# Performance work log

Hardware: AMD Instinct MI355X
Metric: run time of the kernel (lower is better)

## Reference

```python
import jax, jax.numpy as jnp
import numpy as np

PRE_TOPK = 10000   # hardcoded score.topk(10000) in the torch module
TOPK = 100         # final detections kept per image
IOU_THR = 0.7


def cxcywh_to_xyxy(b):
    cx, cy, w, h = jnp.split(b, 4, axis=-1)
    return jnp.concatenate([cx - 0.5 * w, cy - 0.5 * h, cx + 0.5 * w, cy + 0.5 * h], axis=-1)


def iou_one_vs_all(box, boxes):
    # box: [4], boxes: [N,4] (xyxy). torchvision box_iou semantics (no degenerate clamp on areas).
    lt = jnp.maximum(box[:2], boxes[:, :2])
    rb = jnp.minimum(box[2:], boxes[:, 2:])
    wh = jnp.clip(rb - lt, 0.0)
    inter = wh[:, 0] * wh[:, 1]
    a1 = (box[2] - box[0]) * (box[3] - box[1])
    a2 = (boxes[:, 2] - boxes[:, 0]) * (boxes[:, 3] - boxes[:, 1])
    return inter / (a1 + a2 - inter)


def nms_keep_single(boxes, scores, labels):
    # batched (class-wise) NMS via the coordinate-offset trick, then greedy suppression.
    # boxes [N,4], scores [N], labels [N] int. Returns indices of kept boxes, [TOPK],
    # in descending-score order (matches torchvision batched_nms + [:topk]).
    offset = labels.astype(boxes.dtype) * (boxes.max() + 1.0)
    obox = boxes + offset[:, None]

    def step(live, _):
        i = jnp.argmax(live)                      # highest remaining score
        iou = iou_one_vs_all(obox[i], obox)       # [N]
        live = jnp.where(iou > IOU_THR, -jnp.inf, live)  # suppress (includes self, iou=1)
        return live, i

    _, keep = jax.lax.scan(step, scores, None, length=TOPK)
    return keep


def setup_inputs() -> dict:
    key = jax.random.key(0)
    k1, k2, k3 = jax.random.split(key, 3)
    pred_logits = jax.random.normal(k1, (8, 900, 91), dtype=jnp.float32)
    pred_boxes = jax.random.uniform(k2, (8, 900, 4), dtype=jnp.float32)  # cxcywh in [0,1]
    # realistic (h, w) image sizes ~ [600, 1400]
    target_sizes = 600.0 + 800.0 * jax.random.uniform(k3, (8, 2), dtype=jnp.float32)
    return {"pred_logits": pred_logits, "pred_boxes": pred_boxes, "target_sizes": target_sizes}


def reference(pred_logits, pred_boxes, target_sizes):
    bs, nq, nc = pred_logits.shape
    prob = jax.nn.sigmoid(pred_logits).reshape(bs, nq * nc)
    # pre-topk 10000 over flattened (query, class) scores
    top_scores, top_idx = jax.lax.top_k(prob, PRE_TOPK)   # [bs, PRE_TOPK]
    box_idx = top_idx // nc
    labels = top_idx % nc

    xyxy = cxcywh_to_xyxy(pred_boxes)                     # [bs, nq, 4]
    img_h, img_w = target_sizes[:, 0], target_sizes[:, 1]
    scale = jnp.stack([img_w, img_h, img_w, img_h], axis=1)  # [bs, 4]
    xyxy = xyxy * scale[:, None, :]
    boxes = jnp.take_along_axis(xyxy, box_idx[..., None], axis=1)  # [bs, PRE_TOPK, 4]

    keep = jax.vmap(nms_keep_single)(boxes, top_scores, labels)    # [bs, TOPK]

    out_scores = jnp.take_along_axis(top_scores, keep, axis=1)
    out_labels = jnp.take_along_axis(labels, keep, axis=1)
    out_boxes = jnp.take_along_axis(boxes, keep[..., None], axis=1)
    return out_scores, out_labels, out_boxes
```

## Files before the change

kernel.cpp:

```cpp
#include <hip/hip_runtime.h>
#include <cstdint>
#include <cstddef>

#define NQ 900
#define NC 91
#define NFLAT (NQ * NC)
#define NF4 (NFLAT / 4)
#define BS 8
#define PRE_TOPK 10000
#define TOPK 100
#define IOU_THR 0.7f
#define NT 1024
#define NWAVES 16
#define NCAND 256
#define HEADZ 2.55078125f
#define HEADCAP 768

__device__ __forceinline__ unsigned int mono_u(float z) {
    unsigned int b = __float_as_uint(z);
    return b ^ ((unsigned int)((int)b >> 31) | 0x80000000u);
}
__device__ __forceinline__ float inv_mono(unsigned int u) {
    unsigned int b = (u & 0x80000000u) ? (u ^ 0x80000000u) : ~u;
    return __uint_as_float(b);
}
__device__ __forceinline__ unsigned long long make_key(unsigned int u, int i) {
    return ((unsigned long long)u << 17) | (unsigned long long)(131071 - i);
}

extern "C" __global__ __launch_bounds__(NT)
void k_fused(const float* __restrict__ logits,
             const float* __restrict__ pboxes,
             const float* __restrict__ tsizes,
             float* __restrict__ out) {
    __shared__ unsigned long long sPool[PRE_TOPK];
    __shared__ unsigned long long sSup[1024];
    __shared__ float4 sBox[NQ];
    __shared__ unsigned long long sHead[HEADCAP];
    __shared__ unsigned long long sTop[NCAND];
    __shared__ float4 sOB[NCAND];
    __shared__ float sOar[NCAND];
    __shared__ unsigned long long sKeepW[4];
    __shared__ float sKx1[TOPK], sKy1[TOPK], sKx2[TOPK], sKy2[TOPK], sKa[TOPK];
    __shared__ float sFirst[6];
    __shared__ float sRedF[NWAVES];
    __shared__ int sWTot[NWAVES], sWSuf[NWAVES];
    __shared__ int sFlag, sKept, sPos, sNK, sHC;
    __shared__ float sBmax;

    const int b = blockIdx.x;
    const int tid = threadIdx.x;
    const int wid = tid >> 6, lane = tid & 63;
    const float* lg = logits + (size_t)b * NFLAT;
    const float* bx = pboxes + (size_t)b * NQ * 4;
    const float img_h = tsizes[b * 2 + 0], img_w = tsizes[b * 2 + 1];
    const unsigned long long laneLT = (1ULL << lane) - 1ULL;

    if (tid < HEADCAP) sHead[tid] = 0ULL;
    if (tid == 0) { sFlag = 0; sKept = 0; sPos = 0; sNK = 0; sHC = 0; }
    {
        float lmax = -3.4e38f;
        if (tid < NQ) {
            const float4 bb = ((const float4*)bx)[tid];
            float4 sb;
            sb.x = (bb.x - 0.5f * bb.z) * img_w;
            sb.y = (bb.y - 0.5f * bb.w) * img_h;
            sb.z = (bb.x + 0.5f * bb.z) * img_w;
            sb.w = (bb.y + 0.5f * bb.w) * img_h;
            sBox[tid] = sb;
            lmax = fmaxf(fmaxf(sb.x, sb.y), fmaxf(sb.z, sb.w));
        }
        for (int off = 32; off >= 1; off >>= 1)
            lmax = fmaxf(lmax, __shfl_xor(lmax, off, 64));
        if (lane == 0) sRedF[wid] = lmax;
    }
    __syncthreads();

    for (int jj = 0; jj < 5; ++jj) {
        float4 v[4]; bool hv[4];
        #pragma unroll
        for (int u = 0; u < 4; ++u) {
            const int j = tid + (4 * jj + u) * NT;
            hv[u] = (j < NF4);
            v[u] = ((const float4*)lg)[hv[u] ? j : (NF4 - 1)];
        }
        #pragma unroll
        for (int u = 0; u < 4; ++u) {
            const int j = tid + (4 * jj + u) * NT;
            const bool c0 = hv[u] && (v[u].x >= HEADZ);
            const bool c1 = hv[u] && (v[u].y >= HEADZ);
            const bool c2 = hv[u] && (v[u].z >= HEADZ);
            const bool c3 = hv[u] && (v[u].w >= HEADZ);
            const unsigned long long m0 = __ballot(c0), m1 = __ballot(c1),
                                     m2 = __ballot(c2), m3 = __ballot(c3);
            const int p0 = __popcll(m0), p1 = __popcll(m1), p2 = __popcll(m2);
            const int n = p0 + p1 + p2 + __popcll(m3);
            int base = 0;
            if (lane == 0 && n) base = atomicAdd(&sHC, n);
            base = __shfl(base, 0, 64);
            if (c0) { const int o = base + __popcll(m0 & laneLT);
                      if (o < HEADCAP) sHead[o] = make_key(mono_u(v[u].x), 4 * j); }
            if (c1) { const int o = base + p0 + __popcll(m1 & laneLT);
                      if (o < HEADCAP) sHead[o] = make_key(mono_u(v[u].y), 4 * j + 1); }
            if (c2) { const int o = base + p0 + p1 + __popcll(m2 & laneLT);
                      if (o < HEADCAP) sHead[o] = make_key(mono_u(v[u].z), 4 * j + 2); }
            if (c3) { const int o = base + p0 + p1 + p2 + __popcll(m3 & laneLT);
                      if (o < HEADCAP) sHead[o] = make_key(mono_u(v[u].w), 4 * j + 3); }
        }
    }
    __syncthreads();

    {
        const int hcRaw = sHC;
        if (tid == 0 && (hcRaw < NCAND || hcRaw > HEADCAP)) sFlag = 1;
        const int hc = hcRaw < HEADCAP ? hcRaw : HEADCAP;
        if (tid < hc) {
            const unsigned long long k = sHead[tid];
            int r = 0;
            const int hp = (hc + 7) & ~7;
            for (int q = 0; q < hp; q += 8) {
                #pragma unroll
                for (int u = 0; u < 8; ++u) r += (sHead[q + u] > k) ? 1 : 0;
            }
            if (r < NCAND) sTop[r] = k;
        }
    }
    __syncthreads();
    int bad = sFlag;

    if (!bad && tid < NCAND) {
        float mm = sRedF[0];
        #pragma unroll
        for (int q = 1; q < NWAVES; ++q) mm = fmaxf(mm, sRedF[q]);
        const unsigned long long k = sTop[tid];
        const int i = 131071 - (int)(k & 0x1FFFFULL);
        const int bi = i / NC, l = i - bi * NC;
        const float4 sb = sBox[bi];
        const float o = (float)l * (mm + 1.0f);
        float4 ob;
        ob.x = sb.x + o; ob.y = sb.y + o; ob.z = sb.z + o; ob.w = sb.w + o;
        sOB[tid] = ob;
        sOar[tid] = (ob.z - ob.x) * (ob.w - ob.y);
    }
    __syncthreads();

    if (!bad) {
        const int w = wid & 3;
        const int r0 = (wid >> 2) << 6;
        const int cj = (w << 6) + lane;
        const float4 cb = sOB[cj];
        const float car = sOar[cj];
        for (int t = 0; t < 64; ++t) {
            const int i = r0 + t;
            const float4 rb = sOB[i];
            const float ra = sOar[i];
            float iw = fminf(rb.z, cb.z) - fmaxf(rb.x, cb.x);
            float ih = fminf(rb.w, cb.w) - fmaxf(rb.y, cb.y);
            iw = fmaxf(iw, 0.f); ih = fmaxf(ih, 0.f);
            const float inter = iw * ih;
            const bool sup = inter > IOU_THR * (ra + car - inter);
            const unsigned long long bits = __ballot(sup);
            if (lane == 0) sSup[(i << 2) | w] = bits;
        }
    }
    __syncthreads();

    if (!bad && wid == 0) {
        unsigned long long live = (lane < 4) ? ~0ULL : 0ULL;
        unsigned long long keepW = 0ULL;
        int kept = 0;
        const int myw = lane & 3;
        for (int ch = 0; ch < 4 && kept < TOPK; ++ch) {
            unsigned long long cur = __shfl(live, ch, 64);
            unsigned long long acc = 0ULL;
            #pragma unroll 8
            for (int bit = 0; bit < 64; ++bit) {
                const int i = (ch << 6) | bit;
                const unsigned long long rowC = sSup[(i << 2) | ch];
                const unsigned long long rowM = sSup[(i << 2) | myw];
                if ((cur >> bit) & 1ULL) {
                    cur &= ~rowC;
                    acc |= rowM;
                    if (lane == ch) keepW |= 1ULL << bit;
                }
            }
            if (lane < 4) live &= ~acc;
            int c = __popcll(keepW);
            for (int off = 32; off >= 1; off >>= 1) c += __shfl_xor(c, off, 64);
            kept = c;
        }
        if (lane < 4) sKeepW[lane] = keepW;
        if (lane == 0) sNK = kept;
    }
    __syncthreads();
    if (tid == 0 && sFlag == 0) {
        if (sNK < TOPK) sFlag = 1; else sKept = TOPK;
    }
    __syncthreads();
    bad = sFlag;

    if (!bad && tid < NCAND) {
        const int w = tid >> 6;
        const unsigned long long m = sKeepW[w];
        if ((m >> (tid & 63)) & 1ULL) {
            int rank = __popcll(m & ((1ULL << (tid & 63)) - 1ULL));
            for (int ww = 0; ww < w; ++ww) rank += __popcll(sKeepW[ww]);
            if (rank < TOPK) {
                const unsigned long long k = sTop[tid];
                const int i = 131071 - (int)(k & 0x1FFFFULL);
                const int bi = i / NC, l = i - bi * NC;
                const float4 sb = sBox[bi];
                const float z = inv_mono((unsigned int)(k >> 17));
                const int oi = b * TOPK + rank;
                out[oi] = 1.0f / (1.0f + expf(-z));
                out[BS * TOPK + oi] = (float)l;
                out[2 * BS * TOPK + oi * 4 + 0] = sb.x;
                out[2 * BS * TOPK + oi * 4 + 1] = sb.y;
                out[2 * BS * TOPK + oi * 4 + 2] = sb.z;
                out[2 * BS * TOPK + oi * 4 + 3] = sb.w;
            }
        }
    }

    if (bad) {
        unsigned long long lo = 0, hi = (1ULL << 49) - 1;
        while (lo < hi) {
            const unsigned long long mid = lo + ((hi - lo + 1) >> 1);
            int c = 0;
            for (int j = tid; j < NF4; j += NT) {
                const float4 v = ((const float4*)lg)[j];
                const float zv[4] = { v.x, v.y, v.z, v.w };
                #pragma unroll
                for (int q = 0; q < 4; ++q)
                    c += (make_key(mono_u(zv[q]), 4 * j + q) >= mid) ? 1 : 0;
            }
            for (int off = 32; off >= 1; off >>= 1) c += __shfl_xor(c, off, 64);
            if (lane == 0) sWTot[wid] = c;
            __syncthreads();
            if (tid == 0) {
                int a = 0;
                for (int w = 0; w < NWAVES; ++w) a += sWTot[w];
                sPos = a;
            }
            __syncthreads();
            if (sPos >= PRE_TOPK) lo = mid; else hi = mid - 1;
            __syncthreads();
        }
        if (tid == 0) sPos = 0;
        __syncthreads();
        for (int j = tid; j < NF4; j += NT) {
            const float4 v = ((const float4*)lg)[j];
            const float zv[4] = { v.x, v.y, v.z, v.w };
            #pragma unroll
            for (int q = 0; q < 4; ++q) {
                const unsigned long long k = make_key(mono_u(zv[q]), 4 * j + q);
                const bool cand = k >= lo;
                const unsigned long long mask = __ballot(cand);
                int pos = 0;
                if (lane == 0 && mask) pos = atomicAdd(&sPos, __popcll(mask));
                pos = __shfl(pos, 0, 64);
                if (cand) sPool[pos + __popcll(mask & laneLT)] = k;
            }
        }
        __syncthreads();
        {
            unsigned long long stash[10]; int spp[10]; int ns = 0;
            for (int p = tid; p < PRE_TOPK; p += NT) {
                const unsigned long long k = sPool[p];
                int r = 0;
                for (int q = 0; q < PRE_TOPK; ++q) r += (sPool[q] > k) ? 1 : 0;
                if (ns < 10) { stash[ns] = k; spp[ns] = r; ++ns; }
            }
            __syncthreads();
            for (int q = 0; q < ns; ++q) sPool[spp[q]] = stash[q];
        }
        __syncthreads();
        float lmax = -3.4e38f;
        for (int p = tid; p < PRE_TOPK; p += NT) {
            const int i = 131071 - (int)(sPool[p] & 0x1FFFFULL);
            const float4 sb = sBox[i / NC];
            lmax = fmaxf(lmax, fmaxf(fmaxf(sb.x, sb.y), fmaxf(sb.z, sb.w)));
        }
        for (int off = 32; off >= 1; off >>= 1)
            lmax = fmaxf(lmax, __shfl_xor(lmax, off, 64));
        if (lane == 0) sRedF[wid] = lmax;
        __syncthreads();
        if (tid == 0) {
            float mm = sRedF[0];
            for (int k2 = 1; k2 < NWAVES; ++k2) mm = fmaxf(mm, sRedF[k2]);
            sBmax = mm;
        }
        __syncthreads();
        const float offc = sBmax + 1.0f;
        if (wid == 0) {
            int kept = 0;
            for (int base = 0; base < PRE_TOPK && kept < TOPK; base += 64) {
                const int c = base + lane;
                const bool valid = c < PRE_TOPK;
                const unsigned long long k = valid ? sPool[c] : 0ULL;
                const int i = valid ? (131071 - (int)(k & 0x1FFFFULL)) : 0;
                const int bi = i / NC, l = i - bi * NC;
                const float4 sb = sBox[bi];
                const float o = (float)l * offc;
                const float ox1 = sb.x + o, oy1 = sb.y + o, ox2 = sb.z + o, oy2 = sb.w + o;
                const float ar = (ox2 - ox1) * (oy2 - oy1);
                bool alive = valid;
                for (int jj = 0; jj < kept; ++jj) {
                    float iw = fminf(sKx2[jj], ox2) - fmaxf(sKx1[jj], ox1);
                    float ih = fminf(sKy2[jj], oy2) - fmaxf(sKy1[jj], oy1);
                    iw = fmaxf(iw, 0.f); ih = fmaxf(ih, 0.f);
                    const float inter = iw * ih;
                    if (inter > IOU_THR * (sKa[jj] + ar - inter)) alive = false;
                }
                unsigned long long mask = __ballot(alive);
                while (mask != 0ULL && kept < TOPK) {
                    const int s = __ffsll((unsigned long long)mask) - 1;
                    const float px1 = __shfl(ox1, s, 64);
                    const float py1 = __shfl(oy1, s, 64);
                    const float px2 = __shfl(ox2, s, 64);
                    const float py2 = __shfl(oy2, s, 64);
                    const float pa  = __shfl(ar,  s, 64);
                    if (lane == s) {
                        sKx1[kept] = ox1; sKy1[kept] = oy1; sKx2[kept] = ox2;
                        sKy2[kept] = oy2; sKa[kept] = ar;
                        const int oi = b * TOPK + kept;
                        const float z = inv_mono((unsigned int)(k >> 17));
                        const float sc = 1.0f / (1.0f + expf(-z));
                        out[oi] = sc;
                        out[BS * TOPK + oi] = (float)l;
                        out[2 * BS * TOPK + oi * 4 + 0] = sb.x;
                        out[2 * BS * TOPK + oi * 4 + 1] = sb.y;
                        out[2 * BS * TOPK + oi * 4 + 2] = sb.z;
                        out[2 * BS * TOPK + oi * 4 + 3] = sb.w;
                        if (kept == 0) { sFirst[0] = sc; sFirst[1] = (float)l;
                                         sFirst[2] = sb.x; sFirst[3] = sb.y;
                                         sFirst[4] = sb.z; sFirst[5] = sb.w; }
                    }
                    ++kept;
                    if (alive) {
                        float iw = fminf(px2, ox2) - fmaxf(px1, ox1);
                        float ih = fminf(py2, oy2) - fmaxf(py1, oy1);
                        iw = fmaxf(iw, 0.f); ih = fmaxf(ih, 0.f);
                        const float inter = iw * ih;
                        if (inter > IOU_THR * (pa + ar - inter)) alive = false;
                    }
                    mask = __ballot(alive);
                }
            }
            if (lane == 0) sKept = kept;
        }
        __syncthreads();
    }

    for (int t = sKept + tid; t < TOPK; t += NT) {
        const int oi = b * TOPK + t;
        out[oi] = sFirst[0];
        out[BS * TOPK + oi] = sFirst[1];
        out[2 * BS * TOPK + oi * 4 + 0] = sFirst[2];
        out[2 * BS * TOPK + oi * 4 + 1] = sFirst[3];
        out[2 * BS * TOPK + oi * 4 + 2] = sFirst[4];
        out[2 * BS * TOPK + oi * 4 + 3] = sFirst[5];
    }
}

extern "C" void kernel_launch(void* const* d_in, const int* in_sizes, int n_in,
                              void* d_out, int out_size, void* d_ws, size_t ws_size,
                              hipStream_t stream) {
    const float* logits = (const float*)d_in[0];
    const float* pboxes = (const float*)d_in[1];
    const float* ts     = (const float*)d_in[2];
    (void)d_ws; (void)ws_size;
    hipLaunchKernelGGL(k_fused, dim3(BS), dim3(NT), 0, stream,
                       logits, pboxes, ts, (float*)d_out);
}
```

Measured before the change: 91.37 us.

## Split logit threshold sweep into a separate multi-block kernel across slices

Moves the full pass over the 8x81900 logits out of the single-block-per-image kernel into a pre-kernel that uses 32 slices per image (256 blocks). Each slice compacts above-threshold keys into workspace, and the tail kernel prefix-sums the slice counts and gathers the keys into the head buffer. This spreads the memory-bound sweep over many CUs instead of 8, at the cost of an extra launch and a workspace round trip. If workspace is missing or a slice overflows, it falls back to the existing bad path.

```diff
diff --git a/kernel.cpp b/kernel.cpp
--- a/kernel.cpp
+++ b/kernel.cpp
@@ -15,6 +15,13 @@
 #define NCAND 256
 #define HEADZ 2.55078125f
 #define HEADCAP 768
+#define NSL 32
+#define SLCAP 64
+#define K1T 256
+
+#define CNT_OFF 0
+#define KEY_OFF 1024
+#define WS_REQ ((size_t)KEY_OFF + (size_t)BS * NSL * SLCAP * 8)
 
 __device__ __forceinline__ unsigned int mono_u(float z) {
     unsigned int b = __float_as_uint(z);
@@ -28,11 +35,53 @@
     return ((unsigned long long)u << 17) | (unsigned long long)(131071 - i);
 }
 
+extern "C" __global__ __launch_bounds__(K1T)
+void k_sweep(const float* __restrict__ logits, void* __restrict__ ws) {
+    __shared__ unsigned long long keys[SLCAP];
+    __shared__ int cnt;
+    const int sl = blockIdx.x, b = blockIdx.y;
+    const int tid = threadIdx.x, lane = tid & 63;
+    const unsigned long long laneLT = (1ULL << lane) - 1ULL;
+    if (tid == 0) cnt = 0;
+    __syncthreads();
+    const float* lg = logits + (size_t)b * NFLAT;
+    const int j0 = (sl * NF4) / NSL, j1 = ((sl + 1) * NF4) / NSL;
+    for (int j = j0 + tid; j < j1; j += K1T) {
+        const float4 v = ((const float4*)lg)[j];
+        const bool c0 = v.x >= HEADZ, c1 = v.y >= HEADZ,
+                   c2 = v.z >= HEADZ, c3 = v.w >= HEADZ;
+        const unsigned long long m0 = __ballot(c0), m1 = __ballot(c1),
+                                 m2 = __ballot(c2), m3 = __ballot(c3);
+        const int p0 = __popcll(m0), p1 = __popcll(m1), p2 = __popcll(m2);
+        const int n = p0 + p1 + p2 + __popcll(m3);
+        int base = 0;
+        if (lane == 0 && n) base = atomicAdd(&cnt, n);
+        base = __shfl(base, 0, 64);
+        if (c0) { const int o = base + __popcll(m0 & laneLT);
+                  if (o < SLCAP) keys[o] = make_key(mono_u(v.x), 4 * j); }
+        if (c1) { const int o = base + p0 + __popcll(m1 & laneLT);
+                  if (o < SLCAP) keys[o] = make_key(mono_u(v.y), 4 * j + 1); }
+        if (c2) { const int o = base + p0 + p1 + __popcll(m2 & laneLT);
+                  if (o < SLCAP) keys[o] = make_key(mono_u(v.z), 4 * j + 2); }
+        if (c3) { const int o = base + p0 + p1 + p2 + __popcll(m3 & laneLT);
+                  if (o < SLCAP) keys[o] = make_key(mono_u(v.w), 4 * j + 3); }
+    }
+    __syncthreads();
+    const int n = cnt;
+    unsigned long long* kw = (unsigned long long*)((char*)ws + KEY_OFF)
+                             + ((size_t)b * NSL + sl) * SLCAP;
+    const int nw = n < SLCAP ? n : SLCAP;
+    for (int i = tid; i < nw; i += K1T) kw[i] = keys[i];
+    if (tid == 0) ((unsigned int*)((char*)ws + CNT_OFF))[b * NSL + sl] = (unsigned int)n;
+}
+
 extern "C" __global__ __launch_bounds__(NT)
-void k_fused(const float* __restrict__ logits,
-             const float* __restrict__ pboxes,
-             const float* __restrict__ tsizes,
-             float* __restrict__ out) {
+void k_tail(const float* __restrict__ logits,
+            const float* __restrict__ pboxes,
+            const float* __restrict__ tsizes,
+            float* __restrict__ out,
+            const void* __restrict__ ws,
+            const int forceBad) {
     __shared__ unsigned long long sPool[PRE_TOPK];
     __shared__ unsigned long long sSup[1024];
     __shared__ float4 sBox[NQ];
@@ -45,6 +94,7 @@
     __shared__ float sFirst[6];
     __shared__ float sRedF[NWAVES];
     __shared__ int sWTot[NWAVES], sWSuf[NWAVES];
+    __shared__ int sCnt[NSL], sPre[NSL];
     __shared__ int sFlag, sKept, sPos, sNK, sHC;
     __shared__ float sBmax;
 
@@ -57,7 +107,9 @@
     const unsigned long long laneLT = (1ULL << lane) - 1ULL;
 
     if (tid < HEADCAP) sHead[tid] = 0ULL;
-    if (tid == 0) { sFlag = 0; sKept = 0; sPos = 0; sNK = 0; sHC = 0; }
+    if (tid == 0) { sFlag = forceBad; sKept = 0; sPos = 0; sNK = 0; sHC = 0; }
+    if (tid < NSL && !forceBad)
+        sCnt[tid] = (int)((const unsigned int*)((const char*)ws + CNT_OFF))[b * NSL + tid];
     {
         float lmax = -3.4e38f;
         if (tid < NQ) {
@@ -76,44 +128,36 @@
     }
     __syncthreads();
 
-    for (int jj = 0; jj < 5; ++jj) {
-        float4 v[4]; bool hv[4];
+    if (wid == 0) {
+        int c = (lane < NSL) ? sCnt[lane] : 0;
+        if (lane < NSL && c > SLCAP) sFlag = 1;
+        int v = c;
         #pragma unroll
-        for (int u = 0; u < 4; ++u) {
-            const int j = tid + (4 * jj + u) * NT;
-            hv[u] = (j < NF4);
-            v[u] = ((const float4*)lg)[hv[u] ? j : (NF4 - 1)];
-        }
-        #pragma unroll
-        for (int u = 0; u < 4; ++u) {
-            const int j = tid + (4 * jj + u) * NT;
-            const bool c0 = hv[u] && (v[u].x >= HEADZ);
-            const bool c1 = hv[u] && (v[u].y >= HEADZ);
-            const bool c2 = hv[u] && (v[u].z >= HEADZ);
-            const bool c3 = hv[u] && (v[u].w >= HEADZ);
-            const unsigned long long m0 = __ballot(c0), m1 = __ballot(c1),
-                                     m2 = __ballot(c2), m3 = __ballot(c3);
-            const int p0 = __popcll(m0), p1 = __popcll(m1), p2 = __popcll(m2);
-            const int n = p0 + p1 + p2 + __popcll(m3);
-            int base = 0;
-            if (lane == 0 && n) base = atomicAdd(&sHC, n);
-            base = __shfl(base, 0, 64);
-            if (c0) { const int o = base + __popcll(m0 & laneLT);
-                      if (o < HEADCAP) sHead[o] = make_key(mono_u(v[u].x), 4 * j); }
-            if (c1) { const int o = base + p0 + __popcll(m1 & laneLT);
-                      if (o < HEADCAP) sHead[o] = make_key(mono_u(v[u].y), 4 * j + 1); }
-            if (c2) { const int o = base + p0 + p1 + __popcll(m2 & laneLT);
-                      if (o < HEADCAP) sHead[o] = make_key(mono_u(v[u].z), 4 * j + 2); }
-            if (c3) { const int o = base + p0 + p1 + p2 + __popcll(m3 & laneLT);
-                      if (o < HEADCAP) sHead[o] = make_key(mono_u(v[u].w), 4 * j + 3); }
-        }
-    }
-    __syncthreads();
-
-    {
-        const int hcRaw = sHC;
-        if (tid == 0 && (hcRaw < NCAND || hcRaw > HEADCAP)) sFlag = 1;
-        const int hc = hcRaw < HEADCAP ? hcRaw : HEADCAP;
+        for (int off = 1; off < NSL; off <<= 1) {
+            const int o = __shfl(v, lane - off, 64);
+            if (lane >= off) v += o;
+        }
+        if (lane < NSL) sPre[lane] = v - c;
+        if (lane == NSL - 1) {
+            sHC = v;
+            if (v < NCAND || v > HEADCAP) sFlag = 1;
+        }
+    }
+    __syncthreads();
+    int bad = sFlag;
+
+    if (!bad) {
+        const unsigned long long* kr = (const unsigned long long*)((const char*)ws + KEY_OFF)
+                                       + (size_t)b * NSL * SLCAP;
+        for (int s = wid; s < NSL; s += NWAVES) {
+            const int n = sCnt[s], base = sPre[s];
+            if (lane < n) sHead[base + lane] = kr[s * SLCAP + lane];
+        }
+    }
+    __syncthreads();
+
+    if (!bad) {
+        const int hc = sHC;
         if (tid < hc) {
             const unsigned long long k = sHead[tid];
             int r = 0;
@@ -126,7 +170,6 @@
         }
     }
     __syncthreads();
-    int bad = sFlag;
 
     if (!bad && tid < NCAND) {
         float mm = sRedF[0];
@@ -369,7 +412,13 @@
     const float* logits = (const float*)d_in[0];
     const float* pboxes = (const float*)d_in[1];
     const float* ts     = (const float*)d_in[2];
-    (void)d_ws; (void)ws_size;
-    hipLaunchKernelGGL(k_fused, dim3(BS), dim3(NT), 0, stream,
-                       logits, pboxes, ts, (float*)d_out);
-}
+    if (ws_size >= WS_REQ) {
+        hipLaunchKernelGGL(k_sweep, dim3(NSL, BS), dim3(K1T), 0, stream,
+                           logits, d_ws);
+        hipLaunchKernelGGL(k_tail, dim3(BS), dim3(NT), 0, stream,
+                           logits, pboxes, ts, (float*)d_out, d_ws, 0);
+    } else {
+        hipLaunchKernelGGL(k_tail, dim3(BS), dim3(NT), 0, stream,
+                           logits, pboxes, ts, (float*)d_out, d_ws, 1);
+    }
+}
```

Result: faster. 87.76 us (-4.0%).

## Split threshold sweep into a separate multi-block kernel feeding the NMS tail

Applied to the files above, without the earlier changes.

Moves the logits threshold scan out of the single-block-per-image kernel into a new kernel that uses 8 blocks per image, each compacting and partially ranking its slice's candidates into scratch space in the output buffer. The tail kernel then gathers the per-slice candidates with a prefix sum instead of streaming all logits itself. This spreads the memory-bound scan across many more CUs, at the cost of an extra kernel launch, a round trip through global scratch, and new per-slice capacity limits with a fallback-check for truncated slices.

```diff
diff --git a/kernel.cpp b/kernel.cpp
--- a/kernel.cpp
+++ b/kernel.cpp
@@ -14,7 +14,16 @@
 #define NWAVES 16
 #define NCAND 256
 #define HEADZ 2.55078125f
-#define HEADCAP 768
+#define NSL 8
+#define SCAP 64
+#define LCAP 128
+#define HEADCAP 512
+
+__device__ __forceinline__ int scratch_slot(int b, int i) {
+    if (i < 400) return 2 * BS * TOPK + b * 4 * TOPK + i;
+    if (i < 500) return b * TOPK + (i - 400);
+    return BS * TOPK + b * TOPK + (i - 500);
+}
 
 __device__ __forceinline__ unsigned int mono_u(float z) {
     unsigned int b = __float_as_uint(z);
@@ -28,11 +37,77 @@
     return ((unsigned long long)u << 17) | (unsigned long long)(131071 - i);
 }
 
+extern "C" __global__ __launch_bounds__(256)
+void k_sweep(const float* __restrict__ logits, float* __restrict__ out) {
+    __shared__ unsigned long long cand[LCAP];
+    __shared__ int cnt;
+    const int b = blockIdx.x >> 3, s = blockIdx.x & 7;
+    const int tid = threadIdx.x, lane = tid & 63;
+    const unsigned long long laneLT = (1ULL << lane) - 1ULL;
+    if (tid == 0) cnt = 0;
+    __syncthreads();
+    const float* lg = logits + (size_t)b * NFLAT;
+    const int j0 = (s * NF4) / NSL, j1 = ((s + 1) * NF4) / NSL;
+    for (int g = 0; g < 2; ++g) {
+        float4 v[5]; bool hv[5];
+        #pragma unroll
+        for (int u = 0; u < 5; ++u) {
+            const int j = j0 + tid + (g * 5 + u) * 256;
+            hv[u] = (j < j1);
+            v[u] = ((const float4*)lg)[hv[u] ? j : (NF4 - 1)];
+        }
+        #pragma unroll
+        for (int u = 0; u < 5; ++u) {
+            const int j = j0 + tid + (g * 5 + u) * 256;
+            const bool c0 = hv[u] && (v[u].x >= HEADZ);
+            const bool c1 = hv[u] && (v[u].y >= HEADZ);
+            const bool c2 = hv[u] && (v[u].z >= HEADZ);
+            const bool c3 = hv[u] && (v[u].w >= HEADZ);
+            const unsigned long long m0 = __ballot(c0), m1 = __ballot(c1),
+                                     m2 = __ballot(c2), m3 = __ballot(c3);
+            const int p0 = __popcll(m0), p1 = __popcll(m1), p2 = __popcll(m2);
+            const int n = p0 + p1 + p2 + __popcll(m3);
+            if (n == 0) continue;
+            int base = 0;
+            if (lane == 0) base = atomicAdd(&cnt, n);
+            base = __shfl(base, 0, 64);
+            if (c0) { const int o = base + __popcll(m0 & laneLT);
+                      if (o < LCAP) cand[o] = make_key(mono_u(v[u].x), 4 * j); }
+            if (c1) { const int o = base + p0 + __popcll(m1 & laneLT);
+                      if (o < LCAP) cand[o] = make_key(mono_u(v[u].y), 4 * j + 1); }
+            if (c2) { const int o = base + p0 + p1 + __popcll(m2 & laneLT);
+                      if (o < LCAP) cand[o] = make_key(mono_u(v[u].z), 4 * j + 2); }
+            if (c3) { const int o = base + p0 + p1 + p2 + __popcll(m3 & laneLT);
+                      if (o < LCAP) cand[o] = make_key(mono_u(v[u].w), 4 * j + 3); }
+        }
+    }
+    __syncthreads();
+    const int n = cnt;
+    unsigned int* uout = (unsigned int*)out;
+    if (tid == 0) uout[scratch_slot(b, s)] = (unsigned int)n;
+    if (n <= SCAP) {
+        if (tid < n) {
+            const int idx = 131071 - (int)(cand[tid] & 0x1FFFFULL);
+            uout[scratch_slot(b, 8 + s * SCAP + tid)] = (unsigned int)idx;
+        }
+    } else if (n <= LCAP) {
+        if (tid < n) {
+            const unsigned long long k = cand[tid];
+            int r = 0;
+            for (int q = 0; q < n; ++q) r += (cand[q] > k) ? 1 : 0;
+            if (r < SCAP) {
+                const int idx = 131071 - (int)(k & 0x1FFFFULL);
+                uout[scratch_slot(b, 8 + s * SCAP + r)] = (unsigned int)idx;
+            }
+        }
+    }
+}
+
 extern "C" __global__ __launch_bounds__(NT)
-void k_fused(const float* __restrict__ logits,
-             const float* __restrict__ pboxes,
-             const float* __restrict__ tsizes,
-             float* __restrict__ out) {
+void k_tail(const float* __restrict__ logits,
+            const float* __restrict__ pboxes,
+            const float* __restrict__ tsizes,
+            float* __restrict__ out) {
     __shared__ unsigned long long sPool[PRE_TOPK];
     __shared__ unsigned long long sSup[1024];
     __shared__ float4 sBox[NQ];
@@ -45,6 +120,7 @@
     __shared__ float sFirst[6];
     __shared__ float sRedF[NWAVES];
     __shared__ int sWTot[NWAVES], sWSuf[NWAVES];
+    __shared__ int sCntRaw[NSL], sCnt[NSL], sPre[NSL];
     __shared__ int sFlag, sKept, sPos, sNK, sHC;
     __shared__ float sBmax;
 
@@ -53,11 +129,13 @@
     const int wid = tid >> 6, lane = tid & 63;
     const float* lg = logits + (size_t)b * NFLAT;
     const float* bx = pboxes + (size_t)b * NQ * 4;
+    const unsigned int* uout = (const unsigned int*)out;
     const float img_h = tsizes[b * 2 + 0], img_w = tsizes[b * 2 + 1];
     const unsigned long long laneLT = (1ULL << lane) - 1ULL;
 
     if (tid < HEADCAP) sHead[tid] = 0ULL;
     if (tid == 0) { sFlag = 0; sKept = 0; sPos = 0; sNK = 0; sHC = 0; }
+    if (tid < NSL) sCntRaw[tid] = (int)uout[scratch_slot(b, tid)];
     {
         float lmax = -3.4e38f;
         if (tid < NQ) {
@@ -76,44 +154,37 @@
     }
     __syncthreads();
 
-    for (int jj = 0; jj < 5; ++jj) {
-        float4 v[4]; bool hv[4];
+    if (wid == 0) {
+        const int craw = (lane < NSL) ? sCntRaw[lane] : 0;
+        if (lane < NSL && craw > LCAP) sFlag = 1;
+        const int c = craw < SCAP ? craw : SCAP;
+        int v = c;
         #pragma unroll
-        for (int u = 0; u < 4; ++u) {
-            const int j = tid + (4 * jj + u) * NT;
-            hv[u] = (j < NF4);
-            v[u] = ((const float4*)lg)[hv[u] ? j : (NF4 - 1)];
-        }
-        #pragma unroll
-        for (int u = 0; u < 4; ++u) {
-            const int j = tid + (4 * jj + u) * NT;
-            const bool c0 = hv[u] && (v[u].x >= HEADZ);
-            const bool c1 = hv[u] && (v[u].y >= HEADZ);
-            const bool c2 = hv[u] && (v[u].z >= HEADZ);
-            const bool c3 = hv[u] && (v[u].w >= HEADZ);
-            const unsigned long long m0 = __ballot(c0), m1 = __ballot(c1),
-                                     m2 = __ballot(c2), m3 = __ballot(c3);
-            const int p0 = __popcll(m0), p1 = __popcll(m1), p2 = __popcll(m2);
-            const int n = p0 + p1 + p2 + __popcll(m3);
-            int base = 0;
-            if (lane == 0 && n) base = atomicAdd(&sHC, n);
-            base = __shfl(base, 0, 64);
-            if (c0) { const int o = base + __popcll(m0 & laneLT);
-                      if (o < HEADCAP) sHead[o] = make_key(mono_u(v[u].x), 4 * j); }
-            if (c1) { const int o = base + p0 + __popcll(m1 & laneLT);
-                      if (o < HEADCAP) sHead[o] = make_key(mono_u(v[u].y), 4 * j + 1); }
-            if (c2) { const int o = base + p0 + p1 + __popcll(m2 & laneLT);
-                      if (o < HEADCAP) sHead[o] = make_key(mono_u(v[u].z), 4 * j + 2); }
-            if (c3) { const int o = base + p0 + p1 + p2 + __popcll(m3 & laneLT);
-                      if (o < HEADCAP) sHead[o] = make_key(mono_u(v[u].w), 4 * j + 3); }
-        }
-    }
-    __syncthreads();
-
-    {
-        const int hcRaw = sHC;
-        if (tid == 0 && (hcRaw < NCAND || hcRaw > HEADCAP)) sFlag = 1;
-        const int hc = hcRaw < HEADCAP ? hcRaw : HEADCAP;
+        for (int off = 1; off < NSL; off <<= 1) {
+            const int o = __shfl(v, lane - off, 64);
+            if (lane >= off) v += o;
+        }
+        if (lane < NSL) { sPre[lane] = v - c; sCnt[lane] = c; }
+        if (lane == NSL - 1) {
+            sHC = v;
+            if (v < NCAND) sFlag = 1;
+        }
+    }
+    __syncthreads();
+    int bad = sFlag;
+
+    if (!bad && wid < NSL) {
+        const int n = sCnt[wid], base = sPre[wid];
+        if (lane < n) {
+            const int idx = (int)uout[scratch_slot(b, 8 + wid * SCAP + lane)];
+            const float z = lg[idx];
+            sHead[base + lane] = make_key(mono_u(z), idx);
+        }
+    }
+    __syncthreads();
+
+    if (!bad) {
+        const int hc = sHC;
         if (tid < hc) {
             const unsigned long long k = sHead[tid];
             int r = 0;
@@ -126,7 +197,10 @@
         }
     }
     __syncthreads();
-    int bad = sFlag;
+
+    if (!bad && tid < NSL && sCntRaw[tid] > SCAP) {
+        if (sHead[sPre[tid] + SCAP - 1] > sTop[NCAND - 1]) sFlag = 1;
+    }
 
     if (!bad && tid < NCAND) {
         float mm = sRedF[0];
@@ -370,6 +444,8 @@
     const float* pboxes = (const float*)d_in[1];
     const float* ts     = (const float*)d_in[2];
     (void)d_ws; (void)ws_size;
-    hipLaunchKernelGGL(k_fused, dim3(BS), dim3(NT), 0, stream,
+    hipLaunchKernelGGL(k_sweep, dim3(NSL * BS), dim3(256), 0, stream,
+                       logits, (float*)d_out);
+    hipLaunchKernelGGL(k_tail, dim3(BS), dim3(NT), 0, stream,
                        logits, pboxes, ts, (float*)d_out);
 }
```

Result: no change. 91.15 us (-0.2%).

## Split head-candidate scan across 64 blocks with cooperative grid sync

Applied to the files above, without the earlier changes.

The threshold scan over each image's logits is split into 8 slices, giving 64 blocks in total. Each block gathers candidates above the head threshold into a workspace, then a cooperative grid sync lets the 8 per-image blocks assemble the candidate list from the slices. This targets the serial read of the full 82K-logit array by a single block per image, using otherwise idle CUs. The cost is a cooperative launch, a grid-wide barrier and a global round trip. If the workspace is too small, the kernel falls back to the slow exact path.

```diff
diff --git a/kernel.cpp b/kernel.cpp
--- a/kernel.cpp
+++ b/kernel.cpp
@@ -1,6 +1,9 @@
 #include <hip/hip_runtime.h>
+#include <hip/hip_cooperative_groups.h>
 #include <cstdint>
 #include <cstddef>
+
+namespace cg = cooperative_groups;
 
 #define NQ 900
 #define NC 91
@@ -14,7 +17,13 @@
 #define NWAVES 16
 #define NCAND 256
 #define HEADZ 2.55078125f
-#define HEADCAP 768
+#define NSL 8
+#define LCAP 128
+#define HEADCAP (NSL * LCAP)
+
+#define CNT_OFF 0
+#define KEY_OFF 256
+#define WS_REQ ((size_t)KEY_OFF + (size_t)BS * NSL * LCAP * 8)
 
 __device__ __forceinline__ unsigned int mono_u(float z) {
     unsigned int b = __float_as_uint(z);
@@ -29,10 +38,12 @@
 }
 
 extern "C" __global__ __launch_bounds__(NT)
-void k_fused(const float* __restrict__ logits,
-             const float* __restrict__ pboxes,
-             const float* __restrict__ tsizes,
-             float* __restrict__ out) {
+void k_all(const float* __restrict__ logits,
+           const float* __restrict__ pboxes,
+           const float* __restrict__ tsizes,
+           float* __restrict__ out,
+           void* __restrict__ ws,
+           const int forceBad) {
     __shared__ unsigned long long sPool[PRE_TOPK];
     __shared__ unsigned long long sSup[1024];
     __shared__ float4 sBox[NQ];
@@ -45,19 +56,76 @@
     __shared__ float sFirst[6];
     __shared__ float sRedF[NWAVES];
     __shared__ int sWTot[NWAVES], sWSuf[NWAVES];
-    __shared__ int sFlag, sKept, sPos, sNK, sHC;
+    __shared__ int sCntRaw[NSL], sCnt[NSL], sPre[NSL];
+    __shared__ int sFlag, sKept, sPos, sNK, sHC, sSwCnt;
     __shared__ float sBmax;
-
-    const int b = blockIdx.x;
+    unsigned long long* const cand = sPool;
+
     const int tid = threadIdx.x;
     const int wid = tid >> 6, lane = tid & 63;
+    const unsigned long long laneLT = (1ULL << lane) - 1ULL;
+    unsigned int* const cntw = (unsigned int*)((char*)ws + CNT_OFF);
+    unsigned long long* const keyw = (unsigned long long*)((char*)ws + KEY_OFF);
+
+    if (!forceBad) {
+        const int bb = blockIdx.x >> 3, ss = blockIdx.x & 7;
+        const float* lgs = logits + (size_t)bb * NFLAT;
+        const int j0 = (ss * NF4) / NSL, j1 = ((ss + 1) * NF4) / NSL;
+        if (tid == 0) sSwCnt = 0;
+        __syncthreads();
+        {
+            float4 v[3]; bool hv[3];
+            #pragma unroll
+            for (int u = 0; u < 3; ++u) {
+                const int j = j0 + tid + u * NT;
+                hv[u] = (j < j1);
+                v[u] = ((const float4*)lgs)[hv[u] ? j : (NF4 - 1)];
+            }
+            #pragma unroll
+            for (int u = 0; u < 3; ++u) {
+                const int j = j0 + tid + u * NT;
+                const bool c0 = hv[u] && (v[u].x >= HEADZ);
+                const bool c1 = hv[u] && (v[u].y >= HEADZ);
+                const bool c2 = hv[u] && (v[u].z >= HEADZ);
+                const bool c3 = hv[u] && (v[u].w >= HEADZ);
+                const unsigned long long m0 = __ballot(c0), m1 = __ballot(c1),
+                                         m2 = __ballot(c2), m3 = __ballot(c3);
+                const int p0 = __popcll(m0), p1 = __popcll(m1), p2 = __popcll(m2);
+                const int n = p0 + p1 + p2 + __popcll(m3);
+                if (n == 0) continue;
+                int base = 0;
+                if (lane == 0) base = atomicAdd(&sSwCnt, n);
+                base = __shfl(base, 0, 64);
+                if (c0) { const int o = base + __popcll(m0 & laneLT);
+                          if (o < LCAP) cand[o] = make_key(mono_u(v[u].x), 4 * j); }
+                if (c1) { const int o = base + p0 + __popcll(m1 & laneLT);
+                          if (o < LCAP) cand[o] = make_key(mono_u(v[u].y), 4 * j + 1); }
+                if (c2) { const int o = base + p0 + p1 + __popcll(m2 & laneLT);
+                          if (o < LCAP) cand[o] = make_key(mono_u(v[u].z), 4 * j + 2); }
+                if (c3) { const int o = base + p0 + p1 + p2 + __popcll(m3 & laneLT);
+                          if (o < LCAP) cand[o] = make_key(mono_u(v[u].w), 4 * j + 3); }
+            }
+        }
+        __syncthreads();
+        {
+            const int n = sSwCnt;
+            if (tid == 0) cntw[blockIdx.x] = (unsigned int)n;
+            const int nw = n < LCAP ? n : LCAP;
+            if (tid < nw) keyw[(size_t)blockIdx.x * LCAP + tid] = cand[tid];
+        }
+        __threadfence();
+        cg::this_grid().sync();
+        if (blockIdx.x >= BS) return;
+    }
+
+    const int b = blockIdx.x;
     const float* lg = logits + (size_t)b * NFLAT;
     const float* bx = pboxes + (size_t)b * NQ * 4;
     const float img_h = tsizes[b * 2 + 0], img_w = tsizes[b * 2 + 1];
-    const unsigned long long laneLT = (1ULL << lane) - 1ULL;
-
-    if (tid < HEADCAP) sHead[tid] = 0ULL;
-    if (tid == 0) { sFlag = 0; sKept = 0; sPos = 0; sNK = 0; sHC = 0; }
+
+    sHead[tid] = 0ULL;
+    if (tid == 0) { sFlag = forceBad; sKept = 0; sPos = 0; sNK = 0; sHC = 0; }
+    if (tid < NSL && !forceBad) sCntRaw[tid] = (int)cntw[b * NSL + tid];
     {
         float lmax = -3.4e38f;
         if (tid < NQ) {
@@ -76,44 +144,34 @@
     }
     __syncthreads();
 
-    for (int jj = 0; jj < 5; ++jj) {
-        float4 v[4]; bool hv[4];
+    if (wid == 0) {
+        const int craw = (lane < NSL && !forceBad) ? sCntRaw[lane] : 0;
+        if (lane < NSL && craw > LCAP) sFlag = 1;
+        const int c = craw < LCAP ? craw : LCAP;
+        int v = c;
         #pragma unroll
-        for (int u = 0; u < 4; ++u) {
-            const int j = tid + (4 * jj + u) * NT;
-            hv[u] = (j < NF4);
-            v[u] = ((const float4*)lg)[hv[u] ? j : (NF4 - 1)];
-        }
-        #pragma unroll
-        for (int u = 0; u < 4; ++u) {
-            const int j = tid + (4 * jj + u) * NT;
-            const bool c0 = hv[u] && (v[u].x >= HEADZ);
-            const bool c1 = hv[u] && (v[u].y >= HEADZ);
-            const bool c2 = hv[u] && (v[u].z >= HEADZ);
-            const bool c3 = hv[u] && (v[u].w >= HEADZ);
-            const unsigned long long m0 = __ballot(c0), m1 = __ballot(c1),
-                                     m2 = __ballot(c2), m3 = __ballot(c3);
-            const int p0 = __popcll(m0), p1 = __popcll(m1), p2 = __popcll(m2);
-            const int n = p0 + p1 + p2 + __popcll(m3);
-            int base = 0;
-            if (lane == 0 && n) base = atomicAdd(&sHC, n);
-            base = __shfl(base, 0, 64);
-            if (c0) { const int o = base + __popcll(m0 & laneLT);
-                      if (o < HEADCAP) sHead[o] = make_key(mono_u(v[u].x), 4 * j); }
-            if (c1) { const int o = base + p0 + __popcll(m1 & laneLT);
-                      if (o < HEADCAP) sHead[o] = make_key(mono_u(v[u].y), 4 * j + 1); }
-            if (c2) { const int o = base + p0 + p1 + __popcll(m2 & laneLT);
-                      if (o < HEADCAP) sHead[o] = make_key(mono_u(v[u].z), 4 * j + 2); }
-            if (c3) { const int o = base + p0 + p1 + p2 + __popcll(m3 & laneLT);
-                      if (o < HEADCAP) sHead[o] = make_key(mono_u(v[u].w), 4 * j + 3); }
-        }
-    }
-    __syncthreads();
-
-    {
-        const int hcRaw = sHC;
-        if (tid == 0 && (hcRaw < NCAND || hcRaw > HEADCAP)) sFlag = 1;
-        const int hc = hcRaw < HEADCAP ? hcRaw : HEADCAP;
+        for (int off = 1; off < NSL; off <<= 1) {
+            const int o = __shfl(v, lane - off, 64);
+            if (lane >= off) v += o;
+        }
+        if (lane < NSL) { sPre[lane] = v - c; sCnt[lane] = c; }
+        if (lane == NSL - 1) {
+            sHC = v;
+            if (v < NCAND) sFlag = 1;
+        }
+    }
+    __syncthreads();
+    int bad = sFlag;
+
+    if (!bad) {
+        const int sl = wid >> 1, i = ((wid & 1) << 6) + lane;
+        if (i < sCnt[sl])
+            sHead[sPre[sl] + i] = keyw[(size_t)(b * NSL + sl) * LCAP + i];
+    }
+    __syncthreads();
+
+    if (!bad) {
+        const int hc = sHC;
         if (tid < hc) {
             const unsigned long long k = sHead[tid];
             int r = 0;
@@ -126,7 +184,6 @@
         }
     }
     __syncthreads();
-    int bad = sFlag;
 
     if (!bad && tid < NCAND) {
         float mm = sRedF[0];
@@ -254,12 +311,12 @@
             #pragma unroll
             for (int q = 0; q < 4; ++q) {
                 const unsigned long long k = make_key(mono_u(zv[q]), 4 * j + q);
-                const bool cand = k >= lo;
-                const unsigned long long mask = __ballot(cand);
+                const bool cnd = k >= lo;
+                const unsigned long long mask = __ballot(cnd);
                 int pos = 0;
                 if (lane == 0 && mask) pos = atomicAdd(&sPos, __popcll(mask));
                 pos = __shfl(pos, 0, 64);
-                if (cand) sPool[pos + __popcll(mask & laneLT)] = k;
+                if (cnd) sPool[pos + __popcll(mask & laneLT)] = k;
             }
         }
         __syncthreads();
@@ -369,7 +426,16 @@
     const float* logits = (const float*)d_in[0];
     const float* pboxes = (const float*)d_in[1];
     const float* ts     = (const float*)d_in[2];
-    (void)d_ws; (void)ws_size;
-    hipLaunchKernelGGL(k_fused, dim3(BS), dim3(NT), 0, stream,
-                       logits, pboxes, ts, (float*)d_out);
+    float* outp = (float*)d_out;
+    void* wsp = d_ws;
+    if (ws_size >= WS_REQ) {
+        int forceBad = 0;
+        void* args[] = { (void*)&logits, (void*)&pboxes, (void*)&ts,
+                         (void*)&outp, (void*)&wsp, (void*)&forceBad };
+        hipLaunchCooperativeKernel((const void*)k_all, dim3(NSL * BS), dim3(NT),
+                                   args, 0, stream);
+    } else {
+        hipLaunchKernelGGL(k_all, dim3(BS), dim3(NT), 0, stream,
+                           logits, pboxes, ts, outp, wsp, 1);
+    }
 }
```

Measured after the change: 125.1 us. +36.9%, slower.
